# Kernel tuning notes

Hardware: AMD Instinct MI355X
Metric: run time of the kernel (lower is better)

The kernel has to match this reference:

```python
import jax, jax.numpy as jnp
import numpy as np

B, N, D = 4, 128, 128
EPS = 1e-6

def setup_inputs() -> dict:
    key = jax.random.key(0)
    ks = jax.random.split(key, 10)
    q = jax.random.normal(ks[0], (B, N, D), dtype=jnp.float32)
    mu = jax.random.normal(ks[1], (B, N, 3, D), dtype=jnp.float32)
    Wij = jax.random.normal(ks[2], (B, N, N, 3 * D), dtype=jnp.float32)
    dir_ij = jax.random.normal(ks[3], (B, N, N, 3), dtype=jnp.float32)
    mask_ij = jax.random.uniform(ks[4], (B, N, N), dtype=jnp.float32)
    # RMSNorm weight initialized to zeros (torch code: nn.Parameter(torch.zeros(dim)))
    norm_w = jnp.zeros((D,), dtype=jnp.float32)
    # Dense 1 (GLU variant): Linear(D, 2D)
    s1 = 1.0 / np.sqrt(D)
    W1 = jax.random.uniform(ks[5], (2 * D, D), minval=-s1, maxval=s1, dtype=jnp.float32)
    b1 = jax.random.uniform(ks[6], (2 * D,), minval=-s1, maxval=s1, dtype=jnp.float32)
    # Dense 2: Linear(D, 3D), no activation
    W2 = jax.random.uniform(ks[7], (3 * D, D), minval=-s1, maxval=s1, dtype=jnp.float32)
    b2 = jax.random.uniform(ks[8], (3 * D,), minval=-s1, maxval=s1, dtype=jnp.float32)
    return {"q": q, "mu": mu, "Wij": Wij, "dir_ij": dir_ij, "mask_ij": mask_ij,
            "norm_w": norm_w, "W1": W1, "b1": b1, "W2": W2, "b2": b2}

def reference(q, mu, Wij, dir_ij, mask_ij, norm_w, W1, b1, W2, b2):
    # RMSNorm (fp32, unit offset)
    xf = q.astype(jnp.float32)
    var = jnp.mean(xf * xf, axis=-1, keepdims=True)
    h = xf * jax.lax.rsqrt(var + EPS) * (1.0 + norm_w)
    # Dense(D -> D, GLU with silu) then Dense(D -> 3D)
    y = h @ W1.T + b1                      # (B,N,2D)
    a, g = jnp.split(y, 2, axis=-1)
    h2 = jax.nn.silu(a) * jax.nn.sigmoid(g)
    x = h2 @ W2.T + b2                     # (B,N,3D)
    # pairwise broadcast-multiply: xj over neighbor axis j
    x_inter = Wij * x[:, None, :, :] * mask_ij[..., None]   # (B,N,N,3D)
    dq, dmuR, dmumu = jnp.split(x_inter, 3, axis=-1)        # each (B,N,N,D)
    dq = dq.sum(axis=2)                                     # (B,N,D)
    muj = jnp.swapaxes(mu, -1, -2)[:, None]                 # (B,1,N,D,3)
    dmu = (dmuR[..., None] * dir_ij[:, :, :, None, :]
           + dmumu[..., None] * muj).sum(axis=2)            # (B,N,D,3)
    dmu = jnp.swapaxes(dmu, -1, -2)                         # (B,N,3,D)
    return (q + dq, mu + dmu)
```

## Files before the change

### kernel.cpp

```cpp
#include <hip/hip_runtime.h>

#define B_ 4
#define N_ 128
#define D_ 128

typedef __attribute__((ext_vector_type(2))) unsigned short ushort2v;
typedef __attribute__((ext_vector_type(4))) unsigned short ushort4v;
typedef __attribute__((ext_vector_type(2))) float float2v;
typedef __attribute__((ext_vector_type(4))) float float4v;

__device__ __align__(16) float g_x[B_ * N_ * 3 * D_];
__device__ int g_isfp32;

__device__ __forceinline__ float bf2f(unsigned short u) {
    union { unsigned int i; float f; } v; v.i = ((unsigned int)u) << 16; return v.f;
}
__device__ __forceinline__ unsigned short f2bf(float f) {
    union { float f; unsigned int i; } v; v.f = f;
    unsigned int r = v.i + 0x7fffu + ((v.i >> 16) & 1u);
    return (unsigned short)(r >> 16);
}

template<bool FP32>
__device__ __forceinline__ float ld1(const void* p, size_t i) {
    if (FP32) return ((const float*)p)[i];
    return bf2f(((const unsigned short*)p)[i]);
}
template<bool FP32>
__device__ __forceinline__ float2v ld2(const void* p, size_t i) {
    if (FP32) return *(const float2v*)((const float*)p + i);
    ushort2v u = *(const ushort2v*)((const unsigned short*)p + i);
    float2v r; r.x = bf2f(u.x); r.y = bf2f(u.y); return r;
}
template<bool FP32>
__device__ __forceinline__ float4v ld4(const void* p, size_t i) {
    if (FP32) return *(const float4v*)((const float*)p + i);
    ushort4v u = *(const ushort4v*)((const unsigned short*)p + i);
    float4v r; r.x = bf2f(u.x); r.y = bf2f(u.y); r.z = bf2f(u.z); r.w = bf2f(u.w); return r;
}
template<bool FP32>
__device__ __forceinline__ void st2(void* p, size_t i, float a, float b) {
    if (FP32) { float2v v; v.x = a; v.y = b; *(float2v*)((float*)p + i) = v; }
    else { ushort2v v; v.x = f2bf(a); v.y = f2bf(b); *(ushort2v*)((unsigned short*)p + i) = v; }
}

__global__ void detect_dtype(const unsigned short* __restrict__ q) {
    __shared__ int cnts[256];
    int cnt = 0;
    for (int i = threadIdx.x; i < 4096; i += 256) {
        int e = (q[i] >> 7) & 0xFF;
        cnt += (e >= 0xE0) ? 1 : 0;
    }
    cnts[threadIdx.x] = cnt;
    __syncthreads();
    if (threadIdx.x == 0) {
        int tot = 0;
        for (int k = 0; k < 256; ++k) tot += cnts[k];
        g_isfp32 = (tot >= 16) ? 1 : 0;
    }
}

template<bool FP32>
__global__ __launch_bounds__(128) void k1_mlp(
        const void* __restrict__ q, const void* __restrict__ norm_w,
        const void* __restrict__ W1, const void* __restrict__ b1,
        const void* __restrict__ W2, const void* __restrict__ b2) {
    if ((g_isfp32 != 0) != FP32) return;
    const int row = blockIdx.x;
    const int t   = threadIdx.x;

    __shared__ __align__(16) float hbuf[D_];
    __shared__ __align__(16) float h2buf[D_];
    __shared__ float redbuf[2];

    float v  = ld1<FP32>(q, (size_t)row * D_ + t);
    float ss = v * v;
    #pragma unroll
    for (int off = 32; off > 0; off >>= 1) ss += __shfl_down(ss, off);
    if ((t & 63) == 0) redbuf[t >> 6] = ss;
    __syncthreads();
    float var   = (redbuf[0] + redbuf[1]) * (1.0f / D_);
    float scale = rsqrtf(var + 1e-6f);
    hbuf[t] = v * scale * (1.0f + ld1<FP32>(norm_w, t));
    __syncthreads();

    float ya = ld1<FP32>(b1, t);
    float yg = ld1<FP32>(b1, D_ + t);
    #pragma unroll 8
    for (int c = 0; c < D_ / 4; ++c) {
        float4v hv = *(const float4v*)&hbuf[4 * c];
        float4v a4 = ld4<FP32>(W1, (size_t)t * D_ + 4 * c);
        float4v g4 = ld4<FP32>(W1, (size_t)(D_ + t) * D_ + 4 * c);
        ya += hv.x * a4.x + hv.y * a4.y + hv.z * a4.z + hv.w * a4.w;
        yg += hv.x * g4.x + hv.y * g4.y + hv.z * g4.z + hv.w * g4.w;
    }
    float sa = 1.0f / (1.0f + __expf(-ya));
    float sg = 1.0f / (1.0f + __expf(-yg));
    h2buf[t] = ya * sa * sg;
    __syncthreads();

    float x0 = ld1<FP32>(b2, t);
    float x1 = ld1<FP32>(b2, D_ + t);
    float x2 = ld1<FP32>(b2, 2 * D_ + t);
    #pragma unroll 8
    for (int c = 0; c < D_ / 4; ++c) {
        float4v hv = *(const float4v*)&h2buf[4 * c];
        float4v a4 = ld4<FP32>(W2, (size_t)t * D_ + 4 * c);
        float4v b4 = ld4<FP32>(W2, (size_t)(D_ + t) * D_ + 4 * c);
        float4v c4 = ld4<FP32>(W2, (size_t)(2 * D_ + t) * D_ + 4 * c);
        x0 += hv.x * a4.x + hv.y * a4.y + hv.z * a4.z + hv.w * a4.w;
        x1 += hv.x * b4.x + hv.y * b4.y + hv.z * b4.z + hv.w * b4.w;
        x2 += hv.x * c4.x + hv.y * c4.y + hv.z * c4.z + hv.w * c4.w;
    }
    float* xrow = g_x + (size_t)row * (3 * D_);
    xrow[t]          = x0;
    xrow[D_ + t]     = x1;
    xrow[2 * D_ + t] = x2;
}

template<bool FP32>
__global__ __launch_bounds__(256) void k2_pair(
        const void* __restrict__ q, const void* __restrict__ mu,
        const void* __restrict__ Wij, const void* __restrict__ dir,
        const void* __restrict__ mask, void* __restrict__ out) {
    if ((g_isfp32 != 0) != FP32) return;
    const int blk = blockIdx.x;
    const int t   = threadIdx.x;
    const int l   = t & 63;
    const int cw  = t >> 6;
    const int d2  = l * 2;

    const size_t bi = (size_t)blk;
    const int    b  = blk >> 7;
    const size_t wbase  = bi * (N_ * 3 * D_);
    const size_t mbase  = bi * N_;
    const size_t dbase  = bi * (N_ * 3);
    const size_t mubase = (size_t)b * (N_ * 3 * D_);
    const float* xb = g_x + (size_t)b * (N_ * 3 * D_);

    float aq0 = 0.f, aq1 = 0.f;
    float am00 = 0.f, am01 = 0.f, am10 = 0.f, am11 = 0.f, am20 = 0.f, am21 = 0.f;

    const int j0 = cw * 32;
    #pragma unroll 4
    for (int jj = 0; jj < 32; ++jj) {
        const int j = j0 + jj;
        const float m  = ld1<FP32>(mask, mbase + j);
        const float e0 = ld1<FP32>(dir, dbase + j * 3 + 0);
        const float e1 = ld1<FP32>(dir, dbase + j * 3 + 1);
        const float e2 = ld1<FP32>(dir, dbase + j * 3 + 2);

        const size_t wj = wbase + (size_t)j * (3 * D_) + d2;
        float2v wq = ld2<FP32>(Wij, wj);
        float2v wR = ld2<FP32>(Wij, wj + D_);
        float2v wm = ld2<FP32>(Wij, wj + 2 * D_);

        const float* xj = xb + (size_t)j * (3 * D_) + d2;
        float2v xq = *(const float2v*)(xj);
        float2v xR = *(const float2v*)(xj + D_);
        float2v xm = *(const float2v*)(xj + 2 * D_);

        const size_t mj = mubase + (size_t)j * (3 * D_) + d2;
        float2v u0 = ld2<FP32>(mu, mj);
        float2v u1 = ld2<FP32>(mu, mj + D_);
        float2v u2 = ld2<FP32>(mu, mj + 2 * D_);

        aq0 += wq.x * xq.x * m;
        aq1 += wq.y * xq.y * m;
        float tR0 = wR.x * xR.x * m, tR1 = wR.y * xR.y * m;
        float tm0 = wm.x * xm.x * m, tm1 = wm.y * xm.y * m;
        am00 += tR0 * e0 + tm0 * u0.x;  am01 += tR1 * e0 + tm1 * u0.y;
        am10 += tR0 * e1 + tm0 * u1.x;  am11 += tR1 * e1 + tm1 * u1.y;
        am20 += tR0 * e2 + tm0 * u2.x;  am21 += tR1 * e2 + tm1 * u2.y;
    }

    __shared__ float2v red[4][4][64];
    float2v t0; t0.x = aq0;  t0.y = aq1;  red[cw][0][l] = t0;
    float2v t1; t1.x = am00; t1.y = am01; red[cw][1][l] = t1;
    float2v t2; t2.x = am10; t2.y = am11; red[cw][2][l] = t2;
    float2v t3; t3.x = am20; t3.y = am21; red[cw][3][l] = t3;
    __syncthreads();

    float2v s  = red[0][cw][l];
    float2v s1 = red[1][cw][l];
    float2v s2 = red[2][cw][l];
    float2v s3 = red[3][cw][l];
    s.x += s1.x + s2.x + s3.x;
    s.y += s1.y + s2.y + s3.y;

    if (cw == 0) {
        const size_t o = bi * D_ + d2;
        float2v qin = ld2<FP32>(q, o);
        st2<FP32>(out, o, qin.x + s.x, qin.y + s.y);
    } else {
        const int c = cw - 1;
        const size_t o = (bi * 3 + (size_t)c) * D_ + d2;
        float2v mi = ld2<FP32>(mu, o);
        st2<FP32>(out, (size_t)(B_ * N_ * D_) + o, mi.x + s.x, mi.y + s.y);
    }
}

extern "C" void kernel_launch(void* const* d_in, const int* in_sizes, int n_in,
                              void* d_out, int out_size, void* d_ws, size_t ws_size,
                              hipStream_t stream) {
    const void* q     = d_in[0];
    const void* mu    = d_in[1];
    const void* Wij   = d_in[2];
    const void* dir   = d_in[3];
    const void* mask  = d_in[4];
    const void* normw = d_in[5];
    const void* W1    = d_in[6];
    const void* b1    = d_in[7];
    const void* W2    = d_in[8];
    const void* b2    = d_in[9];

    detect_dtype<<<1, 256, 0, stream>>>((const unsigned short*)q);

    k1_mlp<false><<<B_ * N_, 128, 0, stream>>>(q, normw, W1, b1, W2, b2);
    k1_mlp<true ><<<B_ * N_, 128, 0, stream>>>(q, normw, W1, b1, W2, b2);
    k2_pair<false><<<B_ * N_, 256, 0, stream>>>(q, mu, Wij, dir, mask, d_out);
    k2_pair<true ><<<B_ * N_, 256, 0, stream>>>(q, mu, Wij, dir, mask, d_out);
}
```

Baseline: 224.1 us.

## Drop dtype detection, specialize to fp32, vectorize pairwise kernel with float4 loads

Removes the bf16/fp32 runtime dtype detection kernel and the duplicate template launches, leaving one fp32 MLP kernel and one pairwise kernel. The MLP kernel moves to 256 threads, with the GLU inputs staged through shared memory and the W2 rows split across threads. The pairwise kernel uses 512 threads with float4 loads over channels and 16 neighbor slices, reduced by a wave shuffle and then shared memory. This is meant to cut launch overhead and raise memory throughput on the large Wij stream, at the cost of no longer supporting bf16 inputs.

```diff
diff --git a/kernel.cpp b/kernel.cpp
--- a/kernel.cpp
+++ b/kernel.cpp
@@ -1,223 +1,172 @@
 #include <hip/hip_runtime.h>
+
 
 #define B_ 4
 #define N_ 128
 #define D_ 128
 
-typedef __attribute__((ext_vector_type(2))) unsigned short ushort2v;
-typedef __attribute__((ext_vector_type(4))) unsigned short ushort4v;
-typedef __attribute__((ext_vector_type(2))) float float2v;
 typedef __attribute__((ext_vector_type(4))) float float4v;
 
 __device__ __align__(16) float g_x[B_ * N_ * 3 * D_];
-__device__ int g_isfp32;
 
-__device__ __forceinline__ float bf2f(unsigned short u) {
-    union { unsigned int i; float f; } v; v.i = ((unsigned int)u) << 16; return v.f;
-}
-__device__ __forceinline__ unsigned short f2bf(float f) {
-    union { float f; unsigned int i; } v; v.f = f;
-    unsigned int r = v.i + 0x7fffu + ((v.i >> 16) & 1u);
-    return (unsigned short)(r >> 16);
-}
+__device__ __forceinline__ float sigm(float x) { return 1.0f / (1.0f + __expf(-x)); }
 
-template<bool FP32>
-__device__ __forceinline__ float ld1(const void* p, size_t i) {
-    if (FP32) return ((const float*)p)[i];
-    return bf2f(((const unsigned short*)p)[i]);
-}
-template<bool FP32>
-__device__ __forceinline__ float2v ld2(const void* p, size_t i) {
-    if (FP32) return *(const float2v*)((const float*)p + i);
-    ushort2v u = *(const ushort2v*)((const unsigned short*)p + i);
-    float2v r; r.x = bf2f(u.x); r.y = bf2f(u.y); return r;
-}
-template<bool FP32>
-__device__ __forceinline__ float4v ld4(const void* p, size_t i) {
-    if (FP32) return *(const float4v*)((const float*)p + i);
-    ushort4v u = *(const ushort4v*)((const unsigned short*)p + i);
-    float4v r; r.x = bf2f(u.x); r.y = bf2f(u.y); r.z = bf2f(u.z); r.w = bf2f(u.w); return r;
-}
-template<bool FP32>
-__device__ __forceinline__ void st2(void* p, size_t i, float a, float b) {
-    if (FP32) { float2v v; v.x = a; v.y = b; *(float2v*)((float*)p + i) = v; }
-    else { ushort2v v; v.x = f2bf(a); v.y = f2bf(b); *(ushort2v*)((unsigned short*)p + i) = v; }
-}
-
-__global__ void detect_dtype(const unsigned short* __restrict__ q) {
-    __shared__ int cnts[256];
-    int cnt = 0;
-    for (int i = threadIdx.x; i < 4096; i += 256) {
-        int e = (q[i] >> 7) & 0xFF;
-        cnt += (e >= 0xE0) ? 1 : 0;
-    }
-    cnts[threadIdx.x] = cnt;
-    __syncthreads();
-    if (threadIdx.x == 0) {
-        int tot = 0;
-        for (int k = 0; k < 256; ++k) tot += cnts[k];
-        g_isfp32 = (tot >= 16) ? 1 : 0;
-    }
-}
-
-template<bool FP32>
-__global__ __launch_bounds__(128) void k1_mlp(
-        const void* __restrict__ q, const void* __restrict__ norm_w,
-        const void* __restrict__ W1, const void* __restrict__ b1,
-        const void* __restrict__ W2, const void* __restrict__ b2) {
-    if ((g_isfp32 != 0) != FP32) return;
+__global__ __launch_bounds__(256) void k1_mlp(
+        const float* __restrict__ q, const float* __restrict__ norm_w,
+        const float* __restrict__ W1, const float* __restrict__ b1,
+        const float* __restrict__ W2, const float* __restrict__ b2) {
     const int row = blockIdx.x;
     const int t   = threadIdx.x;
 
     __shared__ __align__(16) float hbuf[D_];
     __shared__ __align__(16) float h2buf[D_];
-    __shared__ float redbuf[2];
+    __shared__ float ybuf[2 * D_];
+    __shared__ float red4[4];
 
-    float v  = ld1<FP32>(q, (size_t)row * D_ + t);
+    float v  = (t < D_) ? q[(size_t)row * D_ + t] : 0.0f;
     float ss = v * v;
     #pragma unroll
     for (int off = 32; off > 0; off >>= 1) ss += __shfl_down(ss, off);
-    if ((t & 63) == 0) redbuf[t >> 6] = ss;
+    if ((t & 63) == 0) red4[t >> 6] = ss;
     __syncthreads();
-    float var   = (redbuf[0] + redbuf[1]) * (1.0f / D_);
+    float var   = (red4[0] + red4[1] + red4[2] + red4[3]) * (1.0f / D_);
     float scale = rsqrtf(var + 1e-6f);
-    hbuf[t] = v * scale * (1.0f + ld1<FP32>(norm_w, t));
+    if (t < D_) hbuf[t] = v * scale * (1.0f + norm_w[t]);
     __syncthreads();
 
-    float ya = ld1<FP32>(b1, t);
-    float yg = ld1<FP32>(b1, D_ + t);
+    float y = b1[t];
+    const float4v* wr = (const float4v*)(W1 + (size_t)t * D_);
     #pragma unroll 8
     for (int c = 0; c < D_ / 4; ++c) {
-        float4v hv = *(const float4v*)&hbuf[4 * c];
-        float4v a4 = ld4<FP32>(W1, (size_t)t * D_ + 4 * c);
-        float4v g4 = ld4<FP32>(W1, (size_t)(D_ + t) * D_ + 4 * c);
-        ya += hv.x * a4.x + hv.y * a4.y + hv.z * a4.z + hv.w * a4.w;
-        yg += hv.x * g4.x + hv.y * g4.y + hv.z * g4.z + hv.w * g4.w;
+        float4v w4 = wr[c];
+        float4v h4 = *(const float4v*)&hbuf[4 * c];
+        y += w4.x * h4.x + w4.y * h4.y + w4.z * h4.z + w4.w * h4.w;
     }
-    float sa = 1.0f / (1.0f + __expf(-ya));
-    float sg = 1.0f / (1.0f + __expf(-yg));
-    h2buf[t] = ya * sa * sg;
+    ybuf[t] = y;
+    __syncthreads();
+    if (t < D_) {
+        float a = ybuf[t], g = ybuf[D_ + t];
+        h2buf[t] = a * sigm(a) * sigm(g);
+    }
     __syncthreads();
 
-    float x0 = ld1<FP32>(b2, t);
-    float x1 = ld1<FP32>(b2, D_ + t);
-    float x2 = ld1<FP32>(b2, 2 * D_ + t);
+    float x0 = b2[t];
+    float x1 = (t < D_) ? b2[2 * D_ + t] : 0.0f;
+    const float4v* w0 = (const float4v*)(W2 + (size_t)t * D_);
+    const float4v* w1 = (const float4v*)(W2 + (size_t)(2 * D_ + (t & (D_ - 1))) * D_);
     #pragma unroll 8
     for (int c = 0; c < D_ / 4; ++c) {
-        float4v hv = *(const float4v*)&h2buf[4 * c];
-        float4v a4 = ld4<FP32>(W2, (size_t)t * D_ + 4 * c);
-        float4v b4 = ld4<FP32>(W2, (size_t)(D_ + t) * D_ + 4 * c);
-        float4v c4 = ld4<FP32>(W2, (size_t)(2 * D_ + t) * D_ + 4 * c);
-        x0 += hv.x * a4.x + hv.y * a4.y + hv.z * a4.z + hv.w * a4.w;
-        x1 += hv.x * b4.x + hv.y * b4.y + hv.z * b4.z + hv.w * b4.w;
-        x2 += hv.x * c4.x + hv.y * c4.y + hv.z * c4.z + hv.w * c4.w;
+        float4v h4 = *(const float4v*)&h2buf[4 * c];
+        float4v a4 = w0[c];
+        x0 += a4.x * h4.x + a4.y * h4.y + a4.z * h4.z + a4.w * h4.w;
+        if (t < D_) {
+            float4v b4 = w1[c];
+            x1 += b4.x * h4.x + b4.y * h4.y + b4.z * h4.z + b4.w * h4.w;
+        }
     }
-    float* xrow = g_x + (size_t)row * (3 * D_);
-    xrow[t]          = x0;
-    xrow[D_ + t]     = x1;
-    xrow[2 * D_ + t] = x2;
+    float* xr = g_x + (size_t)row * (3 * D_);
+    xr[t] = x0;
+    if (t < D_) xr[2 * D_ + t] = x1;
 }
 
-template<bool FP32>
-__global__ __launch_bounds__(256) void k2_pair(
-        const void* __restrict__ q, const void* __restrict__ mu,
-        const void* __restrict__ Wij, const void* __restrict__ dir,
-        const void* __restrict__ mask, void* __restrict__ out) {
-    if ((g_isfp32 != 0) != FP32) return;
-    const int blk = blockIdx.x;
-    const int t   = threadIdx.x;
-    const int l   = t & 63;
-    const int cw  = t >> 6;
-    const int d2  = l * 2;
+__global__ __launch_bounds__(512) void k2_pair(
+        const float* __restrict__ q, const float* __restrict__ mu,
+        const float* __restrict__ Wij, const float* __restrict__ dir,
+        const float* __restrict__ mask, float* __restrict__ out) {
+    const int blk  = blockIdx.x;
+    const int t    = threadIdx.x;
+    const int quad = t & 31;
+    const int js   = t >> 5;
+    const int b    = blk >> 7;
 
-    const size_t bi = (size_t)blk;
-    const int    b  = blk >> 7;
-    const size_t wbase  = bi * (N_ * 3 * D_);
-    const size_t mbase  = bi * N_;
-    const size_t dbase  = bi * (N_ * 3);
-    const size_t mubase = (size_t)b * (N_ * 3 * D_);
-    const float* xb = g_x + (size_t)b * (N_ * 3 * D_);
+    const float* Wb  = Wij  + (size_t)blk * (N_ * 3 * D_);
+    const float* mb  = mask + (size_t)blk * N_;
+    const float* db  = dir  + (size_t)blk * (N_ * 3);
+    const float* mub = mu   + (size_t)b * (N_ * 3 * D_);
+    const float* xb  = g_x  + (size_t)b * (N_ * 3 * D_);
 
-    float aq0 = 0.f, aq1 = 0.f;
-    float am00 = 0.f, am01 = 0.f, am10 = 0.f, am11 = 0.f, am20 = 0.f, am21 = 0.f;
+    float4v aq = {0.f, 0.f, 0.f, 0.f};
+    float4v a0 = {0.f, 0.f, 0.f, 0.f};
+    float4v a1 = {0.f, 0.f, 0.f, 0.f};
+    float4v a2 = {0.f, 0.f, 0.f, 0.f};
 
-    const int j0 = cw * 32;
-    #pragma unroll 4
-    for (int jj = 0; jj < 32; ++jj) {
-        const int j = j0 + jj;
-        const float m  = ld1<FP32>(mask, mbase + j);
-        const float e0 = ld1<FP32>(dir, dbase + j * 3 + 0);
-        const float e1 = ld1<FP32>(dir, dbase + j * 3 + 1);
-        const float e2 = ld1<FP32>(dir, dbase + j * 3 + 2);
+    #pragma unroll 2
+    for (int it = 0; it < 8; ++it) {
+        const int j = it * 16 + js;
+        const float m  = mb[j];
+        const float e0 = db[3 * j + 0];
+        const float e1 = db[3 * j + 1];
+        const float e2 = db[3 * j + 2];
 
-        const size_t wj = wbase + (size_t)j * (3 * D_) + d2;
-        float2v wq = ld2<FP32>(Wij, wj);
-        float2v wR = ld2<FP32>(Wij, wj + D_);
-        float2v wm = ld2<FP32>(Wij, wj + 2 * D_);
+        const size_t base = (size_t)j * (3 * D_) + 4 * quad;
+        float4v wq = *(const float4v*)(Wb + base);
+        float4v wR = *(const float4v*)(Wb + base + D_);
+        float4v wm = *(const float4v*)(Wb + base + 2 * D_);
+        float4v xq = *(const float4v*)(xb + base);
+        float4v xR = *(const float4v*)(xb + base + D_);
+        float4v xm = *(const float4v*)(xb + base + 2 * D_);
+        float4v u0 = *(const float4v*)(mub + base);
+        float4v u1 = *(const float4v*)(mub + base + D_);
+        float4v u2 = *(const float4v*)(mub + base + 2 * D_);
 
-        const float* xj = xb + (size_t)j * (3 * D_) + d2;
-        float2v xq = *(const float2v*)(xj);
-        float2v xR = *(const float2v*)(xj + D_);
-        float2v xm = *(const float2v*)(xj + 2 * D_);
-
-        const size_t mj = mubase + (size_t)j * (3 * D_) + d2;
-        float2v u0 = ld2<FP32>(mu, mj);
-        float2v u1 = ld2<FP32>(mu, mj + D_);
-        float2v u2 = ld2<FP32>(mu, mj + 2 * D_);
-
-        aq0 += wq.x * xq.x * m;
-        aq1 += wq.y * xq.y * m;
-        float tR0 = wR.x * xR.x * m, tR1 = wR.y * xR.y * m;
-        float tm0 = wm.x * xm.x * m, tm1 = wm.y * xm.y * m;
-        am00 += tR0 * e0 + tm0 * u0.x;  am01 += tR1 * e0 + tm1 * u0.y;
-        am10 += tR0 * e1 + tm0 * u1.x;  am11 += tR1 * e1 + tm1 * u1.y;
-        am20 += tR0 * e2 + tm0 * u2.x;  am21 += tR1 * e2 + tm1 * u2.y;
+        #pragma unroll
+        for (int i = 0; i < 4; ++i) {
+            aq[i] += wq[i] * (xq[i] * m);
+            float tR = wR[i] * (xR[i] * m);
+            float tm = wm[i] * (xm[i] * m);
+            a0[i] += tR * e0 + tm * u0[i];
+            a1[i] += tR * e1 + tm * u1[i];
+            a2[i] += tR * e2 + tm * u2[i];
+        }
     }
 
-    __shared__ float2v red[4][4][64];
-    float2v t0; t0.x = aq0;  t0.y = aq1;  red[cw][0][l] = t0;
-    float2v t1; t1.x = am00; t1.y = am01; red[cw][1][l] = t1;
-    float2v t2; t2.x = am10; t2.y = am11; red[cw][2][l] = t2;
-    float2v t3; t3.x = am20; t3.y = am21; red[cw][3][l] = t3;
+    #pragma unroll
+    for (int i = 0; i < 4; ++i) {
+        aq[i] += __shfl_down(aq[i], 32);
+        a0[i] += __shfl_down(a0[i], 32);
+        a1[i] += __shfl_down(a1[i], 32);
+        a2[i] += __shfl_down(a2[i], 32);
+    }
+
+    __shared__ __align__(16) float ws[8][4][D_];
+    const int w = t >> 6, l = t & 63;
+    if (l < 32) {
+        *(float4v*)&ws[w][0][4 * quad] = aq;
+        *(float4v*)&ws[w][1][4 * quad] = a0;
+        *(float4v*)&ws[w][2][4 * quad] = a1;
+        *(float4v*)&ws[w][3][4 * quad] = a2;
+    }
     __syncthreads();
 
-    float2v s  = red[0][cw][l];
-    float2v s1 = red[1][cw][l];
-    float2v s2 = red[2][cw][l];
-    float2v s3 = red[3][cw][l];
-    s.x += s1.x + s2.x + s3.x;
-    s.y += s1.y + s2.y + s3.y;
+    const int comp = t >> 7;
+    const int ch   = t & 127;
+    float s = 0.f;
+    #pragma unroll
+    for (int wv = 0; wv < 8; ++wv) s += ws[wv][comp][ch];
 
-    if (cw == 0) {
-        const size_t o = bi * D_ + d2;
-        float2v qin = ld2<FP32>(q, o);
-        st2<FP32>(out, o, qin.x + s.x, qin.y + s.y);
+    if (comp == 0) {
+        const size_t o = (size_t)blk * D_ + ch;
+        out[o] = q[o] + s;
     } else {
-        const int c = cw - 1;
-        const size_t o = (bi * 3 + (size_t)c) * D_ + d2;
-        float2v mi = ld2<FP32>(mu, o);
-        st2<FP32>(out, (size_t)(B_ * N_ * D_) + o, mi.x + s.x, mi.y + s.y);
+        const size_t o = ((size_t)blk * 3 + (comp - 1)) * D_ + ch;
+        out[(size_t)(B_ * N_ * D_) + o] = mu[o] + s;
     }
 }
 
 extern "C" void kernel_launch(void* const* d_in, const int* in_sizes, int n_in,
                               void* d_out, int out_size, void* d_ws, size_t ws_size,
                               hipStream_t stream) {
-    const void* q     = d_in[0];
-    const void* mu    = d_in[1];
-    const void* Wij   = d_in[2];
-    const void* dir   = d_in[3];
-    const void* mask  = d_in[4];
-    const void* normw = d_in[5];
-    const void* W1    = d_in[6];
-    const void* b1    = d_in[7];
-    const void* W2    = d_in[8];
-    const void* b2    = d_in[9];
+    const float* q     = (const float*)d_in[0];
+    const float* mu    = (const float*)d_in[1];
+    const float* Wij   = (const float*)d_in[2];
+    const float* dir   = (const float*)d_in[3];
+    const float* mask  = (const float*)d_in[4];
+    const float* normw = (const float*)d_in[5];
+    const float* W1    = (const float*)d_in[6];
+    const float* b1    = (const float*)d_in[7];
+    const float* W2    = (const float*)d_in[8];
+    const float* b2    = (const float*)d_in[9];
 
-    detect_dtype<<<1, 256, 0, stream>>>((const unsigned short*)q);
-
-    k1_mlp<false><<<B_ * N_, 128, 0, stream>>>(q, normw, W1, b1, W2, b2);
-    k1_mlp<true ><<<B_ * N_, 128, 0, stream>>>(q, normw, W1, b1, W2, b2);
-    k2_pair<false><<<B_ * N_, 256, 0, stream>>>(q, mu, Wij, dir, mask, d_out);
-    k2_pair<true ><<<B_ * N_, 256, 0, stream>>>(q, mu, Wij, dir, mask, d_out);
+    k1_mlp <<<B_ * N_, 256, 0, stream>>>(q, normw, W1, b1, W2, b2);
+    k2_pair<<<B_ * N_, 512, 0, stream>>>(q, mu, Wij, dir, mask, (float*)d_out);
 }
```

Result: faster. 202.5 us (-9.6%).
